# Performance work log

Hardware: AMD Instinct MI355X
Metric: run time of the kernel (lower is better)

The kernel has to match this reference:

```python
import math
import jax, jax.numpy as jnp
import numpy as np

N = 256  # size (power of 2)
B = 512  # batch
STEEPNESS = 10.0  # cauchy distribution steepness


def _bitonic_network(n):
    # n must be a power of 2; every layer then has exactly n//2 compare-exchanges.
    num_blocks = int(math.log2(n))
    sa_l, sb_l, cmin_l, cmax_l = [], [], [], []
    for block_idx in range(num_blocks):
        for layer_idx in range(block_idx + 1):
            m = 2 ** (block_idx - layer_idx)
            split_a = np.zeros((n // 2, n), np.float32)
            split_b = np.zeros((n // 2, n), np.float32)
            combine_min = np.zeros((n, n // 2), np.float32)
            combine_max = np.zeros((n, n // 2), np.float32)
            count = 0
            for i in range(0, n, 2 * m):
                for j in range(m):
                    ix = i + j
                    a, b = ix, ix + m
                    split_a[count, a] = 1.0
                    split_b[count, b] = 1.0
                    if (ix // 2 ** (block_idx + 1)) % 2 == 1:
                        a, b = b, a
                    combine_min[a, count] = 1.0
                    combine_max[b, count] = 1.0
                    count += 1
            sa_l.append(split_a); sb_l.append(split_b)
            cmin_l.append(combine_min); cmax_l.append(combine_max)
    return (np.stack(sa_l), np.stack(sb_l), np.stack(cmin_l), np.stack(cmax_l))


def setup_inputs() -> dict:
    key = jax.random.key(0)
    vectors = jax.random.normal(key, (B, N), dtype=jnp.float32)
    sa, sb, cmin, cmax = _bitonic_network(N)
    return {
        "vectors": vectors,
        "split_a": jnp.asarray(sa),       # [L, n/2, n]
        "split_b": jnp.asarray(sb),       # [L, n/2, n]
        "combine_min": jnp.asarray(cmin), # [L, n, n/2]
        "combine_max": jnp.asarray(cmax), # [L, n, n/2]
    }


def reference(vectors, split_a, split_b, combine_min, combine_max):
    # Faithful to the given source: x (=vectors) is never updated inside the
    # loop; only the soft permutation matrix X is accumulated and returned.
    Bsz, n = vectors.shape
    X0 = jnp.broadcast_to(jnp.eye(n, dtype=vectors.dtype), (Bsz, n, n))

    def step(X, mats):
        sa, sb, cmin, cmax = mats
        a = vectors @ sa.T  # [B, k]
        b = vectors @ sb.T  # [B, k]
        # cauchy interpolation
        alpha = jnp.arctan(STEEPNESS * (b - a)) / jnp.pi + 0.5  # [B, k]
        aX = jnp.einsum('bij,kj->bik', X, sa)  # [B, n, k]
        bX = jnp.einsum('bij,kj->bik', X, sb)  # [B, n, k]
        al = alpha[:, None, :]
        w_min = al * aX + (1.0 - al) * bX
        w_max = (1.0 - al) * aX + al * bX
        X_new = jnp.einsum('bik,jk->bij', w_max, cmax) + jnp.einsum('bik,jk->bij', w_min, cmin)
        return X_new, None

    X, _ = jax.lax.scan(step, X0, (split_a, split_b, combine_min, combine_max))
    return X
```

## Files before the change

kernel.cpp:

```cpp
#include <hip/hip_runtime.h>
#include <math.h>

typedef float vf4 __attribute__((ext_vector_type(4)));

static constexpr int LLB[36] = {
  0,
  1,0,
  2,1,0,
  3,2,1,0,
  4,3,2,1,0,
  5,4,3,2,1,0,
  6,5,4,3,2,1,0,
  7,6,5,4,3,2,1,0
};
static constexpr int LBLK[36] = {
  0,
  1,1,
  2,2,2,
  3,3,3,3,
  4,4,4,4,4,
  5,5,5,5,5,5,
  6,6,6,6,6,6,6,
  7,7,7,7,7,7,7,7
};

__global__ __launch_bounds__(128) void k_ugen(const float* __restrict__ vec,
                                              float* __restrict__ U) {
  const int b = blockIdx.x;
  const int k = threadIdx.x;
  const float* v = vec + b * 256;
  float* ub = U + (size_t)b * 4608;
  #pragma unroll
  for (int l = 0; l < 36; ++l) {
    const int lb  = LLB[l];
    const int blk = LBLK[l];
    const int m = 1 << lb;
    const int p = ((k >> lb) << (lb + 1)) | (k & (m - 1));
    const int q = p + m;
    const int d = (p >> (blk + 1)) & 1;
    const float alpha =
        atanf(10.0f * (v[q] - v[p])) * 0.3183098861837907f + 0.5f;
    ub[l * 128 + k] = d ? (1.0f - alpha) : alpha;
  }
}

__global__ __launch_bounds__(256) void k_phase1(const float* __restrict__ U,
                                                float* __restrict__ staged) {
  const int b = blockIdx.x;
  const int i = threadIdx.x;
  const int g = i >> 6;
  const int il = i & 63;
  float r[64];
  #pragma unroll
  for (int j = 0; j < 64; ++j) r[j] = (j == il) ? 1.0f : 0.0f;

  const int ubase = __builtin_amdgcn_readfirstlane(b * 4608 + 32 * g);
  #pragma unroll
  for (int l = 0; l < 21; ++l) {
    const int lb = LLB[l];
    const int m = 1 << lb;
    const float* ul = U + ubase + l * 128;
    #pragma unroll
    for (int kl = 0; kl < 32; ++kl) {
      const int p = ((kl >> lb) << (lb + 1)) | (kl & (m - 1));
      const int q = p + m;
      const float u = ul[kl];
      const float t  = r[p] - r[q];
      const float np = fmaf(u, t, r[q]);
      const float nq = fmaf(-u, t, r[p]);
      r[p] = np;
      r[q] = nq;
    }
  }
  float* op = staged + ((size_t)b * 256 + i) * 64;
  #pragma unroll
  for (int t = 0; t < 16; ++t)
    *(float4*)(op + 4 * t) =
        make_float4(r[4*t], r[4*t+1], r[4*t+2], r[4*t+3]);
}

__global__ __launch_bounds__(256) void k_phase23(const float* __restrict__ U,
                                                 const float* __restrict__ staged,
                                                 float* __restrict__ out) {
  const int bg = blockIdx.x;
  const int b = bg >> 2;
  const int g = bg & 3;
  const int c  = threadIdx.x >> 6;
  const int rr = threadIdx.x & 63;
  const int i = g * 64 + rr;
  __shared__ float4 ex4[4096];
  float y[64];

  const int ub = __builtin_amdgcn_readfirstlane(b * 4608);

  {
    const int ap = g >> 1;
    if ((c >> 1) == ap) {
      const float* u21 = U + ub + 21 * 128 + 64 * ap;
      const bool sm = ((c & 1) == (g & 1));
      const float* srp = staged + ((size_t)b * 256 + i) * 64;
      #pragma unroll
      for (int t = 0; t < 16; ++t) {
        const float4 s4 = *(const float4*)(srp + 4 * t);
        const float u0 = u21[4*t+0], u1 = u21[4*t+1];
        const float u2 = u21[4*t+2], u3 = u21[4*t+3];
        y[4*t+0] = s4.x * (sm ? u0 : 1.0f - u0);
        y[4*t+1] = s4.y * (sm ? u1 : 1.0f - u1);
        y[4*t+2] = s4.z * (sm ? u2 : 1.0f - u2);
        y[4*t+3] = s4.w * (sm ? u3 : 1.0f - u3);
      }
    } else {
      #pragma unroll
      for (int j = 0; j < 64; ++j) y[j] = 0.0f;
    }
  }

  const int cb = __builtin_amdgcn_readfirstlane(32 * c);

  #pragma unroll
  for (int l = 22; l < 28; ++l) {
    const int lb = LLB[l];
    const int m = 1 << lb;
    const float* ul = U + ub + l * 128 + cb;
    #pragma unroll
    for (int kl = 0; kl < 32; ++kl) {
      const int p = ((kl >> lb) << (lb + 1)) | (kl & (m - 1));
      const int q = p + m;
      const float u = ul[kl];
      const float t  = y[p] - y[q];
      const float np = fmaf(u, t, y[q]);
      const float nq = fmaf(-u, t, y[p]);
      y[p] = np;
      y[q] = nq;
    }
  }

  #pragma unroll
  for (int t = 0; t < 16; ++t)
    ex4[(c * 16 + t) * 64 + rr] =
        make_float4(y[4*t], y[4*t+1], y[4*t+2], y[4*t+3]);
  __syncthreads();
  {
    const int pc = c ^ 2;
    const float* u28 = U + ub + 28 * 128 + 64 * (c & 1);
    #pragma unroll
    for (int t = 0; t < 16; ++t) {
      const float4 p4 = ex4[(pc * 16 + t) * 64 + rr];
      const float u0 = u28[4*t+0], u1 = u28[4*t+1];
      const float u2 = u28[4*t+2], u3 = u28[4*t+3];
      y[4*t+0] = fmaf(u0, y[4*t+0] - p4.x, p4.x);
      y[4*t+1] = fmaf(u1, y[4*t+1] - p4.y, p4.y);
      y[4*t+2] = fmaf(u2, y[4*t+2] - p4.z, p4.z);
      y[4*t+3] = fmaf(u3, y[4*t+3] - p4.w, p4.w);
    }
  }
  __syncthreads();

  #pragma unroll
  for (int t = 0; t < 16; ++t)
    ex4[(c * 16 + t) * 64 + rr] =
        make_float4(y[4*t], y[4*t+1], y[4*t+2], y[4*t+3]);
  __syncthreads();
  {
    const int pc = c ^ 1;
    const float* u29 = U + ub + 29 * 128 + 64 * (c >> 1);
    #pragma unroll
    for (int t = 0; t < 16; ++t) {
      const float4 p4 = ex4[(pc * 16 + t) * 64 + rr];
      const float u0 = u29[4*t+0], u1 = u29[4*t+1];
      const float u2 = u29[4*t+2], u3 = u29[4*t+3];
      y[4*t+0] = fmaf(u0, y[4*t+0] - p4.x, p4.x);
      y[4*t+1] = fmaf(u1, y[4*t+1] - p4.y, p4.y);
      y[4*t+2] = fmaf(u2, y[4*t+2] - p4.z, p4.z);
      y[4*t+3] = fmaf(u3, y[4*t+3] - p4.w, p4.w);
    }
  }

  #pragma unroll
  for (int l = 30; l < 36; ++l) {
    const int lb = LLB[l];
    const int m = 1 << lb;
    const float* ul = U + ub + l * 128 + cb;
    #pragma unroll
    for (int kl = 0; kl < 32; ++kl) {
      const int p = ((kl >> lb) << (lb + 1)) | (kl & (m - 1));
      const int q = p + m;
      const float u = ul[kl];
      const float t  = y[p] - y[q];
      const float np = fmaf(u, t, y[q]);
      const float nq = fmaf(-u, t, y[p]);
      y[p] = np;
      y[q] = nq;
    }
  }

  __syncthreads();
  #pragma unroll
  for (int t = 0; t < 16; ++t) {
    const int q = c * 16 + t;
    ex4[rr * 64 + (q ^ (rr & 7))] =
        make_float4(y[4*t], y[4*t+1], y[4*t+2], y[4*t+3]);
  }
  __syncthreads();
  {
    float4* out4 = (float4*)out + ((size_t)(b * 256 + g * 64)) * 64;
    const int tid = threadIdx.x;
    #pragma unroll
    for (int it = 0; it < 16; ++it) {
      const int fq = it * 256 + tid;
      const int r = fq >> 6;
      const int q = fq & 63;
      const float4 v4 = ex4[r * 64 + (q ^ (r & 7))];
      __builtin_nontemporal_store(*(const vf4*)&v4, (vf4*)&out4[fq]);
    }
  }
}

extern "C" void kernel_launch(void* const* d_in, const int* in_sizes, int n_in,
                              void* d_out, int out_size, void* d_ws, size_t ws_size,
                              hipStream_t stream) {
  const float* vec = (const float*)d_in[0];
  float* out = (float*)d_out;
  float* U = (float*)d_ws;
  float* staged = U + (size_t)512 * 4608;

  hipLaunchKernelGGL(k_ugen,    dim3(512),  dim3(128), 0, stream, vec, U);
  hipLaunchKernelGGL(k_phase1,  dim3(512),  dim3(256), 0, stream, U, staged);
  hipLaunchKernelGGL(k_phase23, dim3(2048), dim3(256), 0, stream, U, staged, out);
}
```

Measured before the change: 225.9 us.

## Fuse alpha generation into phase-1 kernel and halve shared memory in phase 2/3

Merges the alpha-generation kernel into the first butterfly phase: alphas are computed into shared memory and only layers 21+ are written to global memory, which removes one launch and the global round trip for the early-layer coefficients. The staged intermediate is stored in a coalesced float4 layout. In phase 2/3, non-participating waves skip zero work, and the layer-28 exchange is simplified because one side of it is known to be zero. Exchanges and the output transpose are done in two halves so the LDS buffer can be 32KB instead of 64KB, which should allow more resident blocks per CU at the cost of extra barriers.

After: 186.4 us. 17.5% less time.

```diff
diff --git a/kernel.cpp b/kernel.cpp
--- a/kernel.cpp
+++ b/kernel.cpp
@@ -24,195 +24,232 @@
   7,7,7,7,7,7,7,7
 };
 
-__global__ __launch_bounds__(128) void k_ugen(const float* __restrict__ vec,
-                                              float* __restrict__ U) {
+#define BF(ARR, KL, UU) { \
+  const int p_ = (((KL) >> lb) << (lb + 1)) | ((KL) & (m - 1)); \
+  const int q_ = p_ + m; \
+  const float t_  = ARR[p_] - ARR[q_]; \
+  const float np_ = fmaf((UU), t_, ARR[q_]); \
+  const float nq_ = fmaf(-(UU), t_, ARR[p_]); \
+  ARR[p_] = np_; ARR[q_] = nq_; }
+
+__global__ __launch_bounds__(256) void k_gen1(const float* __restrict__ vec,
+                                              float* __restrict__ U2,
+                                              float4* __restrict__ staged2) {
   const int b = blockIdx.x;
-  const int k = threadIdx.x;
-  const float* v = vec + b * 256;
-  float* ub = U + (size_t)b * 4608;
-  #pragma unroll
-  for (int l = 0; l < 36; ++l) {
-    const int lb  = LLB[l];
-    const int blk = LBLK[l];
-    const int m = 1 << lb;
-    const int p = ((k >> lb) << (lb + 1)) | (k & (m - 1));
-    const int q = p + m;
-    const int d = (p >> (blk + 1)) & 1;
-    const float alpha =
-        atanf(10.0f * (v[q] - v[p])) * 0.3183098861837907f + 0.5f;
-    ub[l * 128 + k] = d ? (1.0f - alpha) : alpha;
-  }
-}
-
-__global__ __launch_bounds__(256) void k_phase1(const float* __restrict__ U,
-                                                float* __restrict__ staged) {
-  const int b = blockIdx.x;
-  const int i = threadIdx.x;
-  const int g = i >> 6;
-  const int il = i & 63;
+  const int tid = threadIdx.x;
+  __shared__ __align__(16) float ub[36 * 128];
+  __shared__ float vv[256];
+  vv[tid] = vec[b * 256 + tid];
+  __syncthreads();
+
+  const int k = tid & 127;
+  if (tid < 128) {
+    #pragma unroll
+    for (int l = 0; l < 18; ++l) {
+      const int lb = LLB[l], blk = LBLK[l];
+      const int m = 1 << lb;
+      const int p = ((k >> lb) << (lb + 1)) | (k & (m - 1));
+      const int q = p + m;
+      const int d = (p >> (blk + 1)) & 1;
+      const float alpha =
+          atanf(10.0f * (vv[q] - vv[p])) * 0.3183098861837907f + 0.5f;
+      ub[l * 128 + k] = d ? (1.0f - alpha) : alpha;
+    }
+  } else {
+    #pragma unroll
+    for (int l = 18; l < 36; ++l) {
+      const int lb = LLB[l], blk = LBLK[l];
+      const int m = 1 << lb;
+      const int p = ((k >> lb) << (lb + 1)) | (k & (m - 1));
+      const int q = p + m;
+      const int d = (p >> (blk + 1)) & 1;
+      const float alpha =
+          atanf(10.0f * (vv[q] - vv[p])) * 0.3183098861837907f + 0.5f;
+      const float u = d ? (1.0f - alpha) : alpha;
+      ub[l * 128 + k] = u;
+      if (l >= 21) U2[b * 1920 + (l - 21) * 128 + k] = u;
+    }
+  }
+  __syncthreads();
+
+  const int g  = tid >> 6;
+  const int il = tid & 63;
   float r[64];
   #pragma unroll
   for (int j = 0; j < 64; ++j) r[j] = (j == il) ? 1.0f : 0.0f;
 
-  const int ubase = __builtin_amdgcn_readfirstlane(b * 4608 + 32 * g);
   #pragma unroll
   for (int l = 0; l < 21; ++l) {
     const int lb = LLB[l];
     const int m = 1 << lb;
-    const float* ul = U + ubase + l * 128;
-    #pragma unroll
-    for (int kl = 0; kl < 32; ++kl) {
-      const int p = ((kl >> lb) << (lb + 1)) | (kl & (m - 1));
-      const int q = p + m;
-      const float u = ul[kl];
-      const float t  = r[p] - r[q];
-      const float np = fmaf(u, t, r[q]);
-      const float nq = fmaf(-u, t, r[p]);
-      r[p] = np;
-      r[q] = nq;
-    }
-  }
-  float* op = staged + ((size_t)b * 256 + i) * 64;
+    const float4* ulv = (const float4*)(ub + l * 128 + 32 * g);
+    #pragma unroll
+    for (int t = 0; t < 8; ++t) {
+      const float4 u4 = ulv[t];
+      BF(r, 4*t+0, u4.x)
+      BF(r, 4*t+1, u4.y)
+      BF(r, 4*t+2, u4.z)
+      BF(r, 4*t+3, u4.w)
+    }
+  }
+
+  float4* sp = staged2 + ((size_t)(b * 4 + g) * 16) * 64 + il;
   #pragma unroll
   for (int t = 0; t < 16; ++t)
-    *(float4*)(op + 4 * t) =
-        make_float4(r[4*t], r[4*t+1], r[4*t+2], r[4*t+3]);
+    sp[t * 64] = make_float4(r[4*t], r[4*t+1], r[4*t+2], r[4*t+3]);
 }
 
-__global__ __launch_bounds__(256) void k_phase23(const float* __restrict__ U,
-                                                 const float* __restrict__ staged,
+__global__ __launch_bounds__(256) void k_phase23(const float* __restrict__ U2,
+                                                 const float4* __restrict__ staged2,
                                                  float* __restrict__ out) {
   const int bg = blockIdx.x;
   const int b = bg >> 2;
   const int g = bg & 3;
   const int c  = threadIdx.x >> 6;
   const int rr = threadIdx.x & 63;
-  const int i = g * 64 + rr;
-  __shared__ float4 ex4[4096];
+  __shared__ float4 ex[2048];
   float y[64];
 
-  const int ub = __builtin_amdgcn_readfirstlane(b * 4608);
+  const int ub2 = __builtin_amdgcn_readfirstlane(b * 1920);
+  const int ap = g >> 1;
+  const bool part = ((c >> 1) == ap);
+  const int cb = __builtin_amdgcn_readfirstlane(32 * c);
+
+  if (part) {
+    const bool sm = ((c & 1) == (g & 1));
+    const float* u21 = U2 + ub2 + 64 * ap;
+    const float4* sp = staged2 + ((size_t)(b * 4 + g) * 16) * 64 + rr;
+    #pragma unroll
+    for (int t = 0; t < 16; ++t) {
+      const float4 s4 = sp[t * 64];
+      const float u0 = u21[4*t+0], u1 = u21[4*t+1];
+      const float u2 = u21[4*t+2], u3 = u21[4*t+3];
+      y[4*t+0] = s4.x * (sm ? u0 : 1.0f - u0);
+      y[4*t+1] = s4.y * (sm ? u1 : 1.0f - u1);
+      y[4*t+2] = s4.z * (sm ? u2 : 1.0f - u2);
+      y[4*t+3] = s4.w * (sm ? u3 : 1.0f - u3);
+    }
+    #pragma unroll
+    for (int l = 22; l < 28; ++l) {
+      const int lb = LLB[l];
+      const int m = 1 << lb;
+      const float* ul = U2 + ub2 + (l - 21) * 128 + cb;
+      #pragma unroll
+      for (int kl = 0; kl < 32; ++kl) {
+        const float u = ul[kl];
+        BF(y, kl, u)
+      }
+    }
+  }
 
   {
-    const int ap = g >> 1;
-    if ((c >> 1) == ap) {
-      const float* u21 = U + ub + 21 * 128 + 64 * ap;
-      const bool sm = ((c & 1) == (g & 1));
-      const float* srp = staged + ((size_t)b * 256 + i) * 64;
+    const float* u28 = U2 + ub2 + 7 * 128 + 64 * (c & 1);
+    if (part) {
+      #pragma unroll
+      for (int t = 0; t < 16; ++t)
+        ex[((c & 1) * 16 + t) * 64 + rr] =
+            make_float4(y[4*t], y[4*t+1], y[4*t+2], y[4*t+3]);
+    }
+    __syncthreads();
+    if (part) {
       #pragma unroll
       for (int t = 0; t < 16; ++t) {
-        const float4 s4 = *(const float4*)(srp + 4 * t);
-        const float u0 = u21[4*t+0], u1 = u21[4*t+1];
-        const float u2 = u21[4*t+2], u3 = u21[4*t+3];
-        y[4*t+0] = s4.x * (sm ? u0 : 1.0f - u0);
-        y[4*t+1] = s4.y * (sm ? u1 : 1.0f - u1);
-        y[4*t+2] = s4.z * (sm ? u2 : 1.0f - u2);
-        y[4*t+3] = s4.w * (sm ? u3 : 1.0f - u3);
+        y[4*t+0] *= u28[4*t+0];
+        y[4*t+1] *= u28[4*t+1];
+        y[4*t+2] *= u28[4*t+2];
+        y[4*t+3] *= u28[4*t+3];
       }
     } else {
       #pragma unroll
-      for (int j = 0; j < 64; ++j) y[j] = 0.0f;
-    }
-  }
-
-  const int cb = __builtin_amdgcn_readfirstlane(32 * c);
-
-  #pragma unroll
-  for (int l = 22; l < 28; ++l) {
-    const int lb = LLB[l];
-    const int m = 1 << lb;
-    const float* ul = U + ub + l * 128 + cb;
-    #pragma unroll
-    for (int kl = 0; kl < 32; ++kl) {
-      const int p = ((kl >> lb) << (lb + 1)) | (kl & (m - 1));
-      const int q = p + m;
-      const float u = ul[kl];
-      const float t  = y[p] - y[q];
-      const float np = fmaf(u, t, y[q]);
-      const float nq = fmaf(-u, t, y[p]);
-      y[p] = np;
-      y[q] = nq;
-    }
-  }
-
-  #pragma unroll
-  for (int t = 0; t < 16; ++t)
-    ex4[(c * 16 + t) * 64 + rr] =
-        make_float4(y[4*t], y[4*t+1], y[4*t+2], y[4*t+3]);
-  __syncthreads();
+      for (int t = 0; t < 16; ++t) {
+        const float4 p4 = ex[((c & 1) * 16 + t) * 64 + rr];
+        y[4*t+0] = fmaf(-u28[4*t+0], p4.x, p4.x);
+        y[4*t+1] = fmaf(-u28[4*t+1], p4.y, p4.y);
+        y[4*t+2] = fmaf(-u28[4*t+2], p4.z, p4.z);
+        y[4*t+3] = fmaf(-u28[4*t+3], p4.w, p4.w);
+      }
+    }
+    __syncthreads();
+  }
+
   {
-    const int pc = c ^ 2;
-    const float* u28 = U + ub + 28 * 128 + 64 * (c & 1);
-    #pragma unroll
-    for (int t = 0; t < 16; ++t) {
-      const float4 p4 = ex4[(pc * 16 + t) * 64 + rr];
-      const float u0 = u28[4*t+0], u1 = u28[4*t+1];
-      const float u2 = u28[4*t+2], u3 = u28[4*t+3];
-      y[4*t+0] = fmaf(u0, y[4*t+0] - p4.x, p4.x);
-      y[4*t+1] = fmaf(u1, y[4*t+1] - p4.y, p4.y);
-      y[4*t+2] = fmaf(u2, y[4*t+2] - p4.z, p4.z);
-      y[4*t+3] = fmaf(u3, y[4*t+3] - p4.w, p4.w);
-    }
-  }
-  __syncthreads();
-
-  #pragma unroll
-  for (int t = 0; t < 16; ++t)
-    ex4[(c * 16 + t) * 64 + rr] =
-        make_float4(y[4*t], y[4*t+1], y[4*t+2], y[4*t+3]);
-  __syncthreads();
-  {
+    const float* u29 = U2 + ub2 + 8 * 128 + 64 * (c >> 1);
     const int pc = c ^ 1;
-    const float* u29 = U + ub + 29 * 128 + 64 * (c >> 1);
-    #pragma unroll
-    for (int t = 0; t < 16; ++t) {
-      const float4 p4 = ex4[(pc * 16 + t) * 64 + rr];
-      const float u0 = u29[4*t+0], u1 = u29[4*t+1];
-      const float u2 = u29[4*t+2], u3 = u29[4*t+3];
-      y[4*t+0] = fmaf(u0, y[4*t+0] - p4.x, p4.x);
-      y[4*t+1] = fmaf(u1, y[4*t+1] - p4.y, p4.y);
-      y[4*t+2] = fmaf(u2, y[4*t+2] - p4.z, p4.z);
-      y[4*t+3] = fmaf(u3, y[4*t+3] - p4.w, p4.w);
-    }
+    #pragma unroll
+    for (int t = 0; t < 8; ++t)
+      ex[(c * 8 + t) * 64 + rr] =
+          make_float4(y[4*t], y[4*t+1], y[4*t+2], y[4*t+3]);
+    __syncthreads();
+    #pragma unroll
+    for (int t = 0; t < 8; ++t) {
+      const float4 p4 = ex[(pc * 8 + t) * 64 + rr];
+      y[4*t+0] = fmaf(u29[4*t+0], y[4*t+0] - p4.x, p4.x);
+      y[4*t+1] = fmaf(u29[4*t+1], y[4*t+1] - p4.y, p4.y);
+      y[4*t+2] = fmaf(u29[4*t+2], y[4*t+2] - p4.z, p4.z);
+      y[4*t+3] = fmaf(u29[4*t+3], y[4*t+3] - p4.w, p4.w);
+    }
+    __syncthreads();
+    #pragma unroll
+    for (int t = 8; t < 16; ++t)
+      ex[(c * 8 + (t - 8)) * 64 + rr] =
+          make_float4(y[4*t], y[4*t+1], y[4*t+2], y[4*t+3]);
+    __syncthreads();
+    #pragma unroll
+    for (int t = 8; t < 16; ++t) {
+      const float4 p4 = ex[(pc * 8 + (t - 8)) * 64 + rr];
+      y[4*t+0] = fmaf(u29[4*t+0], y[4*t+0] - p4.x, p4.x);
+      y[4*t+1] = fmaf(u29[4*t+1], y[4*t+1] - p4.y, p4.y);
+      y[4*t+2] = fmaf(u29[4*t+2], y[4*t+2] - p4.z, p4.z);
+      y[4*t+3] = fmaf(u29[4*t+3], y[4*t+3] - p4.w, p4.w);
+    }
+    __syncthreads();
   }
 
   #pragma unroll
   for (int l = 30; l < 36; ++l) {
     const int lb = LLB[l];
     const int m = 1 << lb;
-    const float* ul = U + ub + l * 128 + cb;
+    const float* ul = U2 + ub2 + (l - 21) * 128 + cb;
     #pragma unroll
     for (int kl = 0; kl < 32; ++kl) {
-      const int p = ((kl >> lb) << (lb + 1)) | (kl & (m - 1));
-      const int q = p + m;
       const float u = ul[kl];
-      const float t  = y[p] - y[q];
-      const float np = fmaf(u, t, y[q]);
-      const float nq = fmaf(-u, t, y[p]);
-      y[p] = np;
-      y[q] = nq;
-    }
-  }
-
-  __syncthreads();
-  #pragma unroll
-  for (int t = 0; t < 16; ++t) {
-    const int q = c * 16 + t;
-    ex4[rr * 64 + (q ^ (rr & 7))] =
-        make_float4(y[4*t], y[4*t+1], y[4*t+2], y[4*t+3]);
-  }
-  __syncthreads();
-  {
-    float4* out4 = (float4*)out + ((size_t)(b * 256 + g * 64)) * 64;
-    const int tid = threadIdx.x;
-    #pragma unroll
-    for (int it = 0; it < 16; ++it) {
-      const int fq = it * 256 + tid;
-      const int r = fq >> 6;
-      const int q = fq & 63;
-      const float4 v4 = ex4[r * 64 + (q ^ (r & 7))];
-      __builtin_nontemporal_store(*(const vf4*)&v4, (vf4*)&out4[fq]);
-    }
+      BF(y, kl, u)
+    }
+  }
+
+  float4* out4 = (float4*)out + ((size_t)(b * 256 + g * 64)) * 64;
+  const int tid = threadIdx.x;
+
+  if (rr < 32) {
+    #pragma unroll
+    for (int t = 0; t < 16; ++t)
+      ex[rr * 64 + ((c * 16 + t) ^ (rr & 7))] =
+          make_float4(y[4*t], y[4*t+1], y[4*t+2], y[4*t+3]);
+  }
+  __syncthreads();
+  #pragma unroll
+  for (int it = 0; it < 8; ++it) {
+    const int fq = it * 256 + tid;
+    const int r_ = fq >> 6;
+    const int q_ = fq & 63;
+    const float4 v4 = ex[r_ * 64 + (q_ ^ (r_ & 7))];
+    __builtin_nontemporal_store(*(const vf4*)&v4, (vf4*)&out4[fq]);
+  }
+  __syncthreads();
+  if (rr >= 32) {
+    #pragma unroll
+    for (int t = 0; t < 16; ++t)
+      ex[(rr - 32) * 64 + ((c * 16 + t) ^ (rr & 7))] =
+          make_float4(y[4*t], y[4*t+1], y[4*t+2], y[4*t+3]);
+  }
+  __syncthreads();
+  #pragma unroll
+  for (int it = 0; it < 8; ++it) {
+    const int fq = it * 256 + tid;
+    const int r_ = fq >> 6;
+    const int q_ = fq & 63;
+    const float4 v4 = ex[r_ * 64 + (q_ ^ (r_ & 7))];
+    __builtin_nontemporal_store(*(const vf4*)&v4, (vf4*)&out4[2048 + fq]);
   }
 }
 
@@ -221,10 +258,9 @@
                               hipStream_t stream) {
   const float* vec = (const float*)d_in[0];
   float* out = (float*)d_out;
-  float* U = (float*)d_ws;
-  float* staged = U + (size_t)512 * 4608;
-
-  hipLaunchKernelGGL(k_ugen,    dim3(512),  dim3(128), 0, stream, vec, U);
-  hipLaunchKernelGGL(k_phase1,  dim3(512),  dim3(256), 0, stream, U, staged);
-  hipLaunchKernelGGL(k_phase23, dim3(2048), dim3(256), 0, stream, U, staged, out);
+  float* U2 = (float*)d_ws;
+  float4* staged2 = (float4*)(U2 + (size_t)512 * 1920);
+
+  hipLaunchKernelGGL(k_gen1,    dim3(512),  dim3(256), 0, stream, vec, U2, staged2);
+  hipLaunchKernelGGL(k_phase23, dim3(2048), dim3(256), 0, stream, U2, staged2, out);
 }
```
